# Performance work log

Hardware: AMD Instinct MI355X
Metric: run time of the kernel (lower is better)

Reference implementation:

```python
import jax, jax.numpy as jnp
import numpy as np

B, P, D, S = 1024, 200, 512, 64  # batch, num prototypes (nall), feat_dim, subdim


def setup_inputs() -> dict:
    key = jax.random.key(0)
    k1, k2, k3 = jax.random.split(key, 3)
    x = jax.random.normal(k1, (B, D), dtype=jnp.float32)
    protos = jax.random.normal(k2, (P, D), dtype=jnp.float32)
    subspaces = jax.random.normal(k3, (P, D, S), dtype=jnp.float32)
    return {"x": x, "protos": protos, "subspaces": subspaces}


def reference(x, protos, subspaces):
    # diff: [B, P, D]
    diff = x[:, None, :] - protos[None, :, :]
    # per-prototype tangent-space projectors: I - U U^T, [P, D, D]
    projectors = jnp.eye(D, dtype=subspaces.dtype) - jnp.einsum(
        'pds,pes->pde', subspaces, subspaces)
    # project diffs and take L2 norm over feature dim -> [B, P]
    proj_diff = jnp.einsum('bpd,pde->bpe', diff, projectors)
    return jnp.linalg.norm(proj_diff, ord=2, axis=-1)
```

## Files before the change

kernel.cpp:

```cpp
#include <hip/hip_runtime.h>
#include <math.h>


#define NB 1024
#define NP 200
#define ND 512
#define NS 64
#define NS5 80

#define OFF_C   0
#define OFF_PN  12800
#define OFF_XN  13000
#define OFF_GB  14024
#define OFF_XB  423624
#define OFF_UB  685768

typedef __attribute__((ext_vector_type(8))) short bf16x8;
typedef __attribute__((ext_vector_type(8))) unsigned short ushort8;
typedef __attribute__((ext_vector_type(4))) float f32x4;

__device__ __forceinline__ unsigned short f2bf(float f) {
  unsigned int u = __float_as_uint(f);
  u += 0x7fffu + ((u >> 16) & 1u);
  return (unsigned short)(u >> 16);
}
__device__ __forceinline__ float bf2f(unsigned short h) {
  return __uint_as_float(((unsigned int)h) << 16);
}
__device__ __forceinline__ void gl_lds16(const void* g, void* l) {
  __builtin_amdgcn_global_load_lds(
      (const __attribute__((address_space(1))) unsigned int*)g,
      (__attribute__((address_space(3))) unsigned int*)l, 16, 0, 0);
}

__global__ __launch_bounds__(256) void k_conv(
    const float* __restrict__ x, const float* __restrict__ protos,
    const float* __restrict__ U, float* __restrict__ ws)
{
  const int bid = blockIdx.x, tid = threadIdx.x;
  if (bid >= 800) {
    const int b = (bid - 800) * 32 + (tid >> 3);
    const int cc = tid & 7;
    const float* src = x + (size_t)b * ND + cc * 64;
    unsigned short* dst = (unsigned short*)(ws + OFF_XB) + (size_t)b * ND + cc * 64;
    float s = 0.f;
#pragma unroll
    for (int i = 0; i < 8; ++i) {
      float4 v0 = *(const float4*)(src + i * 8);
      float4 v1 = *(const float4*)(src + i * 8 + 4);
      ushort8 o;
      o[0]=f2bf(v0.x); o[1]=f2bf(v0.y); o[2]=f2bf(v0.z); o[3]=f2bf(v0.w);
      o[4]=f2bf(v1.x); o[5]=f2bf(v1.y); o[6]=f2bf(v1.z); o[7]=f2bf(v1.w);
      *(ushort8*)(dst + i * 8) = o;
      s += v0.x*v0.x + v0.y*v0.y + v0.z*v0.z + v0.w*v0.w
         + v1.x*v1.x + v1.y*v1.y + v1.z*v1.z + v1.w*v1.w;
    }
    s += __shfl_xor(s, 1); s += __shfl_xor(s, 2); s += __shfl_xor(s, 4);
    if (cc == 0) ws[OFF_XN + b] = s;
    return;
  }
  const int p = bid >> 2, d0 = (bid & 3) * 128;
  __shared__ unsigned short ts[128][66];
#pragma unroll
  for (int i = 0; i < 8; ++i) {
    int row = (tid >> 4) + i * 16;
    int col = (tid & 15) * 4;
    float4 v = *(const float4*)(U + ((size_t)p * ND + d0 + row) * NS + col);
    ts[row][col] = f2bf(v.x); ts[row][col+1] = f2bf(v.y);
    ts[row][col+2] = f2bf(v.z); ts[row][col+3] = f2bf(v.w);
  }
  __syncthreads();
  unsigned short* Ubg = (unsigned short*)(ws + OFF_UB) + (size_t)p * NS5 * ND;
#pragma unroll
  for (int i = 0; i < 4; ++i) {
    int f = tid + i * 256;
    int s = f >> 4, g = f & 15;
    ushort8 o;
#pragma unroll
    for (int j = 0; j < 8; ++j) o[j] = ts[g * 8 + j][s];
    *(ushort8*)(Ubg + (size_t)s * ND + d0 + g * 8) = o;
  }
  if (tid < 16) {
    const float* pr = protos + (size_t)p * ND + d0 + tid * 8;
    float4 v0 = *(const float4*)pr, v1 = *(const float4*)(pr + 4);
    ushort8 o;
    o[0]=f2bf(v0.x); o[1]=f2bf(v0.y); o[2]=f2bf(v0.z); o[3]=f2bf(v0.w);
    o[4]=f2bf(v1.x); o[5]=f2bf(v1.y); o[6]=f2bf(v1.z); o[7]=f2bf(v1.w);
    *(ushort8*)(Ubg + (size_t)64 * ND + d0 + tid * 8) = o;
  }
}

__global__ __launch_bounds__(256) void k_gram(float* __restrict__ ws) {
  const int p = blockIdx.x;
  __shared__ __align__(16) unsigned short ut[NS5 * ND];
  const int tid = threadIdx.x, l = tid & 63, w = tid >> 6;
  const int lm = l & 15, lh = l >> 4;
  const unsigned short* ub =
      (const unsigned short*)(ws + OFF_UB) + (size_t)p * NS5 * ND;
#pragma unroll
  for (int i = 0; i < 20; ++i) {
    int f = tid + i * 256;
    int r = f >> 6;
    int gd = (f & 63) ^ (r & 15);
    *(ushort8*)(ut + (size_t)f * 8) = *(const ushort8*)(ub + (size_t)r * ND + gd * 8);
  }
  __syncthreads();
  const int ntile = (w == 0) ? 6 : 5;
  for (int idx = 0; idx < ntile; ++idx) {
    int tt = (idx == 5) ? 20 : (w + 4 * idx);
    int i1 = (tt == 20) ? 4 : tt / 5;
    int i2 = (tt == 20) ? 4 : tt % 5;
    f32x4 g = {0.f, 0.f, 0.f, 0.f};
#pragma unroll
    for (int ks = 0; ks < 16; ++ks) {
      int sl = (ks * 4 + lh) ^ lm;
      bf16x8 a = *(const bf16x8*)(ut + ((size_t)(i1 * 16 + lm) * 64 + sl) * 8);
      bf16x8 b = *(const bf16x8*)(ut + ((size_t)(i2 * 16 + lm) * 64 + sl) * 8);
      g = __builtin_amdgcn_mfma_f32_16x16x32_bf16(a, b, g, 0, 0, 0);
    }
    int col = i2 * 16 + lm;
    int row0 = i1 * 16 + lh * 4;
    if (i1 < 4 && i2 < 4) {
      unsigned short* Gbg = (unsigned short*)(ws + OFF_GB) + (size_t)p * 4096;
#pragma unroll
      for (int q = 0; q < 4; ++q) Gbg[(size_t)(row0 + q) * 64 + col] = f2bf(g[q]);
    } else if (i1 < 4 && i2 == 4 && lm == 0) {
#pragma unroll
      for (int q = 0; q < 4; ++q) ws[OFF_C + p * 64 + row0 + q] = g[q];
    } else if (tt == 20 && l == 0) {
      ws[OFF_PN + p] = g[0];
    }
  }
}

__global__ __launch_bounds__(256) void k_main(float* __restrict__ ws,
                                              float* __restrict__ out)
{
  const int p = blockIdx.x;
  const int b0 = blockIdx.y * 128;
  __shared__ __align__(16) char smem[58112];
  unsigned short* xs = (unsigned short*)smem;
  unsigned short* us = (unsigned short*)(smem + 32768);
  unsigned short* tb = (unsigned short*)smem;
  unsigned short* gs = (unsigned short*)(smem + 18432);
  float* cs  = (float*)(smem + 57344);
  float* xps = (float*)(smem + 57600);
  const int tid = threadIdx.x, l = tid & 63, w = tid >> 6;
  const int lm = l & 15, lh = l >> 4;

  const unsigned short* Xb = (const unsigned short*)(ws + OFF_XB) + (size_t)b0 * ND;
  const unsigned short* Ub = (const unsigned short*)(ws + OFF_UB) + (size_t)p * NS5 * ND;

  auto stage = [&](int buf, int k0) {
#pragma unroll
    for (int c = 0; c < 4; ++c) {
      int f = w * 256 + c * 64 + l;
      int r = f >> 3, gd = (f & 7) ^ (r & 7);
      gl_lds16(Xb + (size_t)r * ND + k0 + gd * 8,
               xs + ((size_t)buf * 8192 + (w * 256 + c * 64) * 8));
    }
#pragma unroll
    for (int c = 0; c < 3; ++c) {
      int f = w * 192 + c * 64 + l;
      int r = f >> 3, gd = (f & 7) ^ (r & 7);
      gl_lds16(Ub + (size_t)r * ND + k0 + gd * 8,
               us + ((size_t)buf * 6144 + (w * 192 + c * 64) * 8));
    }
  };

  stage(0, 0);
  if (tid < 16)
    *(float4*)(cs + tid * 4) = *(const float4*)(ws + OFF_C + p * 64 + tid * 4);
  asm volatile("s_waitcnt vmcnt(0) lgkmcnt(0)" ::: "memory");
  __builtin_amdgcn_s_barrier();

  f32x4 acc[2][5] = {};
  for (int it = 0; it < 8; ++it) {
    const int buf = it & 1;
    if (it < 7) stage(buf ^ 1, (it + 1) * 64);
    const unsigned short* xb = xs + buf * 8192;
    const unsigned short* ub2 = us + buf * 6144;
#pragma unroll
    for (int ks = 0; ks < 2; ++ks) {
      const int slot = (ks * 4 + lh) ^ (lm & 7);
      bf16x8 a0 = *(const bf16x8*)(xb + (((size_t)((w*2+0)*16 + lm)) * 8 + slot) * 8);
      bf16x8 a1 = *(const bf16x8*)(xb + (((size_t)((w*2+1)*16 + lm)) * 8 + slot) * 8);
#pragma unroll
      for (int j = 0; j < 5; ++j) {
        bf16x8 b = *(const bf16x8*)(ub2 + (((size_t)(j*16 + lm)) * 8 + slot) * 8);
        acc[0][j] = __builtin_amdgcn_mfma_f32_16x16x32_bf16(a0, b, acc[0][j], 0, 0, 0);
        acc[1][j] = __builtin_amdgcn_mfma_f32_16x16x32_bf16(a1, b, acc[1][j], 0, 0, 0);
      }
    }
    asm volatile("s_waitcnt vmcnt(0)" ::: "memory");
    __builtin_amdgcn_s_barrier();
  }

  {
    const unsigned short* Gbg = (const unsigned short*)(ws + OFF_GB) + (size_t)p * 4096;
#pragma unroll
    for (int i = 0; i < 2; ++i) {
      int f = tid + i * 256;
      int r = f >> 3, g = f & 7;
      *(ushort8*)(gs + (size_t)r * 72 + g * 8) =
          *(const ushort8*)(Gbg + (size_t)r * 64 + g * 8);
    }
  }

  float tn[2][4] = {};
#pragma unroll
  for (int i = 0; i < 2; ++i) {
    int rbase = (w * 2 + i) * 16 + lh * 4;
#pragma unroll
    for (int j = 0; j < 5; ++j) {
      f32x4 v = acc[i][j];
      if (j < 4) {
        int col = j * 16 + lm;
        float cj = cs[col];
#pragma unroll
        for (int q = 0; q < 4; ++q) {
          float t = v[q] - cj;
          tn[i][q] += t * t;
          tb[(size_t)(rbase + q) * 72 + col] = f2bf(t);
        }
      } else if (lm == 0) {
#pragma unroll
        for (int q = 0; q < 4; ++q) xps[rbase + q] = v[q];
      }
    }
  }
  __syncthreads();

  f32x4 acc2[2][4] = {};
#pragma unroll
  for (int ks = 0; ks < 2; ++ks) {
#pragma unroll
    for (int i = 0; i < 2; ++i) {
      bf16x8 a = *(const bf16x8*)(tb + (size_t)((w*2+i)*16 + lm) * 72 + ks*32 + lh*8);
#pragma unroll
      for (int j = 0; j < 4; ++j) {
        bf16x8 b = *(const bf16x8*)(gs + (size_t)(j*16 + lm) * 72 + ks*32 + lh*8);
        acc2[i][j] = __builtin_amdgcn_mfma_f32_16x16x32_bf16(a, b, acc2[i][j], 0, 0, 0);
      }
    }
  }

  const float pnv = ws[OFF_PN + p];
#pragma unroll
  for (int i = 0; i < 2; ++i) {
    int rbase = (w * 2 + i) * 16 + lh * 4;
    float tgt[4] = {0.f, 0.f, 0.f, 0.f};
#pragma unroll
    for (int j = 0; j < 4; ++j) {
      int col = j * 16 + lm;
#pragma unroll
      for (int q = 0; q < 4; ++q)
        tgt[q] += acc2[i][j][q] * bf2f(tb[(size_t)(rbase + q) * 72 + col]);
    }
#pragma unroll
    for (int q = 0; q < 4; ++q) {
      float ta = tgt[q], tnv = tn[i][q];
#pragma unroll
      for (int m = 1; m <= 8; m <<= 1) {
        ta += __shfl_xor(ta, m);
        tnv += __shfl_xor(tnv, m);
      }
      tgt[q] = ta; tn[i][q] = tnv;
    }
    if (lm == 0) {
#pragma unroll
      for (int q = 0; q < 4; ++q) {
        int r = rbase + q;
        int bb = b0 + r;
        float qq = ws[OFF_XN + bb] - 2.f * xps[r] + pnv;
        float v = qq - 2.f * tn[i][q] + tgt[q];
        out[(size_t)bb * NP + p] = sqrtf(fmaxf(v, 0.f));
      }
    }
  }
}

extern "C" void kernel_launch(void* const* d_in, const int* in_sizes, int n_in,
                              void* d_out, int out_size, void* d_ws, size_t ws_size,
                              hipStream_t stream) {
  const float* x      = (const float*)d_in[0];
  const float* protos = (const float*)d_in[1];
  const float* U      = (const float*)d_in[2];
  float* out = (float*)d_out;
  float* ws  = (float*)d_ws;

  k_conv<<<dim3(832),     dim3(256), 0, stream>>>(x, protos, U, ws);
  k_gram<<<dim3(NP),      dim3(256), 0, stream>>>(ws);
  k_main<<<dim3(NP, 8),   dim3(256), 0, stream>>>(ws, out);
}
```

Measured before the change: 128.7 us.

## Load MFMA operands directly from global memory instead of LDS double-buffering

The projection GEMM in k_main no longer stages X and U tiles into LDS with global_load_lds double buffering and per-iteration barriers. Each lane now reads its bf16x8 fragments straight from global memory, and the loop is unrolled by two. LDS use drops from about 58KB to 28KB, and the barrier moves to after the main loop. In exchange, U fragments are fetched redundantly by all four waves, and the per-lane 16-byte loads are strided across rows, so the kernel leans on L1/L2 caching rather than coalesced bulk copies.

```diff
diff --git a/kernel.cpp b/kernel.cpp
--- a/kernel.cpp
+++ b/kernel.cpp
@@ -26,11 +26,6 @@
 }
 __device__ __forceinline__ float bf2f(unsigned short h) {
   return __uint_as_float(((unsigned int)h) << 16);
-}
-__device__ __forceinline__ void gl_lds16(const void* g, void* l) {
-  __builtin_amdgcn_global_load_lds(
-      (const __attribute__((address_space(1))) unsigned int*)g,
-      (__attribute__((address_space(3))) unsigned int*)l, 16, 0, 0);
 }
 
 __global__ __launch_bounds__(256) void k_conv(
@@ -138,63 +133,13 @@
 {
   const int p = blockIdx.x;
   const int b0 = blockIdx.y * 128;
-  __shared__ __align__(16) char smem[58112];
-  unsigned short* xs = (unsigned short*)smem;
-  unsigned short* us = (unsigned short*)(smem + 32768);
+  __shared__ __align__(16) char smem[28416];
   unsigned short* tb = (unsigned short*)smem;
   unsigned short* gs = (unsigned short*)(smem + 18432);
-  float* cs  = (float*)(smem + 57344);
-  float* xps = (float*)(smem + 57600);
+  float* cs  = (float*)(smem + 27648);
+  float* xps = (float*)(smem + 27904);
   const int tid = threadIdx.x, l = tid & 63, w = tid >> 6;
   const int lm = l & 15, lh = l >> 4;
-
-  const unsigned short* Xb = (const unsigned short*)(ws + OFF_XB) + (size_t)b0 * ND;
-  const unsigned short* Ub = (const unsigned short*)(ws + OFF_UB) + (size_t)p * NS5 * ND;
-
-  auto stage = [&](int buf, int k0) {
-#pragma unroll
-    for (int c = 0; c < 4; ++c) {
-      int f = w * 256 + c * 64 + l;
-      int r = f >> 3, gd = (f & 7) ^ (r & 7);
-      gl_lds16(Xb + (size_t)r * ND + k0 + gd * 8,
-               xs + ((size_t)buf * 8192 + (w * 256 + c * 64) * 8));
-    }
-#pragma unroll
-    for (int c = 0; c < 3; ++c) {
-      int f = w * 192 + c * 64 + l;
-      int r = f >> 3, gd = (f & 7) ^ (r & 7);
-      gl_lds16(Ub + (size_t)r * ND + k0 + gd * 8,
-               us + ((size_t)buf * 6144 + (w * 192 + c * 64) * 8));
-    }
-  };
-
-  stage(0, 0);
-  if (tid < 16)
-    *(float4*)(cs + tid * 4) = *(const float4*)(ws + OFF_C + p * 64 + tid * 4);
-  asm volatile("s_waitcnt vmcnt(0) lgkmcnt(0)" ::: "memory");
-  __builtin_amdgcn_s_barrier();
-
-  f32x4 acc[2][5] = {};
-  for (int it = 0; it < 8; ++it) {
-    const int buf = it & 1;
-    if (it < 7) stage(buf ^ 1, (it + 1) * 64);
-    const unsigned short* xb = xs + buf * 8192;
-    const unsigned short* ub2 = us + buf * 6144;
-#pragma unroll
-    for (int ks = 0; ks < 2; ++ks) {
-      const int slot = (ks * 4 + lh) ^ (lm & 7);
-      bf16x8 a0 = *(const bf16x8*)(xb + (((size_t)((w*2+0)*16 + lm)) * 8 + slot) * 8);
-      bf16x8 a1 = *(const bf16x8*)(xb + (((size_t)((w*2+1)*16 + lm)) * 8 + slot) * 8);
-#pragma unroll
-      for (int j = 0; j < 5; ++j) {
-        bf16x8 b = *(const bf16x8*)(ub2 + (((size_t)(j*16 + lm)) * 8 + slot) * 8);
-        acc[0][j] = __builtin_amdgcn_mfma_f32_16x16x32_bf16(a0, b, acc[0][j], 0, 0, 0);
-        acc[1][j] = __builtin_amdgcn_mfma_f32_16x16x32_bf16(a1, b, acc[1][j], 0, 0, 0);
-      }
-    }
-    asm volatile("s_waitcnt vmcnt(0)" ::: "memory");
-    __builtin_amdgcn_s_barrier();
-  }
 
   {
     const unsigned short* Gbg = (const unsigned short*)(ws + OFF_GB) + (size_t)p * 4096;
@@ -205,7 +150,34 @@
       *(ushort8*)(gs + (size_t)r * 72 + g * 8) =
           *(const ushort8*)(Gbg + (size_t)r * 64 + g * 8);
     }
-  }
+    if (tid < 16)
+      *(float4*)(cs + tid * 4) = *(const float4*)(ws + OFF_C + p * 64 + tid * 4);
+  }
+
+  const unsigned short* Xb = (const unsigned short*)(ws + OFF_XB) + (size_t)b0 * ND;
+  const unsigned short* Ub = (const unsigned short*)(ws + OFF_UB) + (size_t)p * NS5 * ND;
+  const unsigned short* xr0 = Xb + (size_t)((w * 2 + 0) * 16 + lm) * ND;
+  const unsigned short* xr1 = Xb + (size_t)((w * 2 + 1) * 16 + lm) * ND;
+  const unsigned short* ur  = Ub + (size_t)lm * ND;
+
+  f32x4 acc[2][5] = {};
+#pragma unroll 2
+  for (int it = 0; it < 8; ++it) {
+    const int k0 = it * 64;
+#pragma unroll
+    for (int ks = 0; ks < 2; ++ks) {
+      const int kc = k0 + ks * 32 + lh * 8;
+      bf16x8 a0 = *(const bf16x8*)(xr0 + kc);
+      bf16x8 a1 = *(const bf16x8*)(xr1 + kc);
+#pragma unroll
+      for (int j = 0; j < 5; ++j) {
+        bf16x8 b = *(const bf16x8*)(ur + (size_t)j * 16 * ND + kc);
+        acc[0][j] = __builtin_amdgcn_mfma_f32_16x16x32_bf16(a0, b, acc[0][j], 0, 0, 0);
+        acc[1][j] = __builtin_amdgcn_mfma_f32_16x16x32_bf16(a1, b, acc[1][j], 0, 0, 0);
+      }
+    }
+  }
+  __syncthreads();
 
   float tn[2][4] = {};
 #pragma unroll
@@ -229,7 +201,6 @@
       }
     }
   }
-  __syncthreads();
 
   f32x4 acc2[2][4] = {};
 #pragma unroll
@@ -289,7 +260,7 @@
   float* out = (float*)d_out;
   float* ws  = (float*)d_ws;
 
-  k_conv<<<dim3(832),     dim3(256), 0, stream>>>(x, protos, U, ws);
-  k_gram<<<dim3(NP),      dim3(256), 0, stream>>>(ws);
-  k_main<<<dim3(NP, 8),   dim3(256), 0, stream>>>(ws, out);
-}
+  k_conv<<<dim3(832),   dim3(256), 0, stream>>>(x, protos, U, ws);
+  k_gram<<<dim3(NP),    dim3(256), 0, stream>>>(ws);
+  k_main<<<dim3(NP, 8), dim3(256), 0, stream>>>(ws, out);
+}
```

Measured after the change: 181.3 us. +40.9%, slower.
